# Optimization experiments

Hardware: AMD Instinct MI355X
Metric: run time of the kernel (lower is better)

Reference implementation:

```python
import jax, jax.numpy as jnp
import numpy as np

D_MODEL = 1024
NUM_HEADS = 16
D_K = D_MODEL // NUM_HEADS
D_FF = 4096
EPS = 1e-5


def layer_norm(x, gamma, beta):
    mu = jnp.mean(x, axis=-1, keepdims=True)
    var = jnp.mean(jnp.square(x - mu), axis=-1, keepdims=True)
    return (x - mu) * jax.lax.rsqrt(var + EPS) * gamma + beta


def setup_inputs() -> dict:
    key = jax.random.key(0)
    ks = jax.random.split(key, 12)
    B, S = 2, 2048
    s_attn = 1.0 / np.sqrt(D_MODEL)
    s_ff1 = 1.0 / np.sqrt(D_MODEL)
    s_ff2 = 1.0 / np.sqrt(D_FF)
    return {
        "x": jax.random.normal(ks[0], (B, S, D_MODEL), dtype=jnp.float32),
        "mask": jnp.ones((B, 1, 1, S), dtype=jnp.int32),
        "Wq": jax.random.normal(ks[1], (D_MODEL, D_MODEL), jnp.float32) * s_attn,
        "bq": jnp.zeros((D_MODEL,), jnp.float32),
        "Wk": jax.random.normal(ks[2], (D_MODEL, D_MODEL), jnp.float32) * s_attn,
        "bk": jnp.zeros((D_MODEL,), jnp.float32),
        "Wv": jax.random.normal(ks[3], (D_MODEL, D_MODEL), jnp.float32) * s_attn,
        "bv": jnp.zeros((D_MODEL,), jnp.float32),
        "Wo": jax.random.normal(ks[4], (D_MODEL, D_MODEL), jnp.float32) * s_attn,
        "bo": jnp.zeros((D_MODEL,), jnp.float32),
        "W1": jax.random.normal(ks[5], (D_MODEL, D_FF), jnp.float32) * s_ff1,
        "b1": jnp.zeros((D_FF,), jnp.float32),
        "W2": jax.random.normal(ks[6], (D_FF, D_MODEL), jnp.float32) * s_ff2,
        "b2": jnp.zeros((D_MODEL,), jnp.float32),
        "g1": jnp.ones((D_MODEL,), jnp.float32),
        "be1": jnp.zeros((D_MODEL,), jnp.float32),
        "g2": jnp.ones((D_MODEL,), jnp.float32),
        "be2": jnp.zeros((D_MODEL,), jnp.float32),
    }


def reference(x, mask, Wq, bq, Wk, bk, Wv, bv, Wo, bo, W1, b1, W2, b2, g1, be1, g2, be2):
    B, S, _ = x.shape

    def split_heads(t):  # [B,S,D] -> [B,H,S,Dk]
        return t.reshape(B, S, NUM_HEADS, D_K).transpose(0, 2, 1, 3)

    q = split_heads(x @ Wq + bq)
    k = split_heads(x @ Wk + bk)
    v = split_heads(x @ Wv + bv)

    scores = jnp.einsum("bhsd,bhtd->bhst", q, k) / np.sqrt(D_K)
    scores = jnp.where(mask == 0, -jnp.inf, scores)
    probs = jax.nn.softmax(scores, axis=-1)
    attn = jnp.einsum("bhst,bhtd->bhsd", probs, v)
    attn = attn.transpose(0, 2, 1, 3).reshape(B, S, D_MODEL)
    attn_out = attn @ Wo + bo

    h = layer_norm(x + attn_out, g1, be1)  # dropout=0 (eval)
    ff = jax.nn.relu(h @ W1 + b1) @ W2 + b2
    out = layer_norm(h + ff, g2, be2)
    return out
```

## Files before the change

kernel.cpp:

```cpp
#include <hip/hip_runtime.h>
#include <hip/hip_bf16.h>

#define DMODEL 1024
#define DFF    4096
#define NHEAD  16
#define DK     64
#define SEQ    2048
#define BATCH  2
#define MTOT   (BATCH*SEQ)
#define LOG2E  1.44269504f
#define MREF_L2E (-14.0f * 1.44269504f)

typedef __attribute__((ext_vector_type(8))) short bf16x8;
typedef __attribute__((ext_vector_type(4))) float f32x4;

typedef const unsigned int __attribute__((address_space(1)))* gas_u32p;
typedef unsigned int __attribute__((address_space(3)))* las_u32p;

__device__ __forceinline__ void gload_lds16(const void* g, void* l) {
  __builtin_amdgcn_global_load_lds((gas_u32p)g, (las_u32p)l, 16, 0, 0);
}

__device__ __forceinline__ f32x4 mfma16(bf16x8 a, bf16x8 b, f32x4 c) {
  return __builtin_amdgcn_mfma_f32_16x16x32_bf16(a, b, c, 0, 0, 0);
}

__device__ __forceinline__ unsigned short bf16bits(float f) {
  union { __hip_bfloat16 h; unsigned short u; } c; c.h = __float2bfloat16(f); return c.u;
}

__device__ __forceinline__ unsigned pack_bf16(float a, float b) {
  return (unsigned)bf16bits(a) | ((unsigned)bf16bits(b) << 16);
}

__device__ __forceinline__ void store_bf16x4(__hip_bfloat16* p, float a, float b, float c, float d) {
  union { __hip_bfloat16 h[4]; ushort4 u; } pk;
  pk.h[0] = __float2bfloat16(a); pk.h[1] = __float2bfloat16(b);
  pk.h[2] = __float2bfloat16(c); pk.h[3] = __float2bfloat16(d);
  *(ushort4*)p = pk.u;
}

__global__ __launch_bounds__(256) void cvt_bf16_kernel(const float* __restrict__ in,
                                                       __hip_bfloat16* __restrict__ out, int n) {
  int i = (blockIdx.x * 256 + threadIdx.x) * 4;
  if (i >= n) return;
  float4 v = *(const float4*)(in + i);
  store_bf16x4(out + i, v.x, v.y, v.z, v.w);
}

__global__ __launch_bounds__(256) void transpose_cvt_kernel(const float* __restrict__ in,
                                                            __hip_bfloat16* __restrict__ out,
                                                            int R, int C) {
  __shared__ float tile[32][33];
  int tx = threadIdx.x, ty = threadIdx.y;
  int c0 = blockIdx.x * 32, r0 = blockIdx.y * 32;
  #pragma unroll
  for (int j = 0; j < 32; j += 8)
    tile[ty + j][tx] = in[(size_t)(r0 + ty + j) * C + c0 + tx];
  __syncthreads();
  #pragma unroll
  for (int j = 0; j < 32; j += 8)
    out[(size_t)(c0 + ty + j) * R + r0 + tx] = __float2bfloat16(tile[tx][ty + j]);
}

__global__ __launch_bounds__(256)
void transpose4_cvt_kernel(const float* __restrict__ A0, const float* __restrict__ A1,
                           const float* __restrict__ A2, const float* __restrict__ A3,
                           __hip_bfloat16* __restrict__ O0, __hip_bfloat16* __restrict__ O1,
                           __hip_bfloat16* __restrict__ O2, __hip_bfloat16* __restrict__ O3) {
  const float* in; __hip_bfloat16* out;
  switch (blockIdx.z) {
    case 0: in = A0; out = O0; break;
    case 1: in = A1; out = O1; break;
    case 2: in = A2; out = O2; break;
    default: in = A3; out = O3; break;
  }
  __shared__ float tile[32][33];
  int tx = threadIdx.x, ty = threadIdx.y;
  int c0 = blockIdx.x * 32, r0 = blockIdx.y * 32;
  #pragma unroll
  for (int j = 0; j < 32; j += 8)
    tile[ty + j][tx] = in[(size_t)(r0 + ty + j) * DMODEL + c0 + tx];
  __syncthreads();
  #pragma unroll
  for (int j = 0; j < 32; j += 8)
    out[(size_t)(c0 + ty + j) * DMODEL + r0 + tx] = __float2bfloat16(tile[tx][ty + j]);
}

template<int MI, int NT>
__device__ __forceinline__ void gemm_core(const __hip_bfloat16* __restrict__ A,
                                          const __hip_bfloat16* __restrict__ Bt,
                                          int K, size_t blockM, size_t blockN,
                                          __hip_bfloat16* As, __hip_bfloat16* Bs,
                                          f32x4 (&acc)[MI][4]) {
  constexpr int BM = (NT / 128) * MI * 16;
  constexpr int RP = NT / 8;
  const int tid = threadIdx.x;
  const int w = tid >> 6, l = tid & 63;
  const int q = l >> 4, ln = l & 15;
  const int m_off = (w >> 1) * MI * 16, n_off = (w & 1) * 64;
  const int lr = l >> 3, lc = (l & 7) ^ lr;

  for (int k0 = 0; k0 < K; k0 += 64) {
    __syncthreads();
    #pragma unroll
    for (int t = 0; t < 128 / RP; ++t) {
      int ra = t * RP + w * 8;
      gload_lds16(Bt + (blockN + ra + lr) * (size_t)K + k0 + lc * 8, Bs + ra * 64);
      if (t < BM / RP)
        gload_lds16(A + (blockM + ra + lr) * (size_t)K + k0 + lc * 8, As + ra * 64);
    }
    __syncthreads();
    #pragma unroll
    for (int kk = 0; kk < 2; ++kk) {
      bf16x8 af[MI], bfr[4];
      #pragma unroll
      for (int mi = 0; mi < MI; ++mi) {
        int R = m_off + mi * 16 + ln;
        int p = (kk * 4 + q) ^ (R & 7);
        af[mi] = *(const bf16x8*)(As + R * 64 + p * 8);
      }
      #pragma unroll
      for (int ni = 0; ni < 4; ++ni) {
        int R = n_off + ni * 16 + ln;
        int p = (kk * 4 + q) ^ (R & 7);
        bfr[ni] = *(const bf16x8*)(Bs + R * 64 + p * 8);
      }
      #pragma unroll
      for (int mi = 0; mi < MI; ++mi)
        #pragma unroll
        for (int ni = 0; ni < 4; ++ni)
          acc[mi][ni] = mfma16(af[mi], bfr[ni], acc[mi][ni]);
    }
  }
}

template<int MI, int NT, int RELU, int WRITE_BF16>
__global__ __launch_bounds__(NT)
void gemm_bt_kernel(const __hip_bfloat16* __restrict__ A, const __hip_bfloat16* __restrict__ Bt,
                    const float* __restrict__ bias, float* __restrict__ Cf,
                    __hip_bfloat16* __restrict__ Cb, int M, int N, int K) {
  constexpr int BM = (NT / 128) * MI * 16;
  __shared__ __align__(16) __hip_bfloat16 As[BM * 64];
  __shared__ __align__(16) __hip_bfloat16 Bs[128 * 64];
  f32x4 acc[MI][4] = {};
  const size_t blockM = blockIdx.y * (size_t)BM, blockN = blockIdx.x * 128;
  gemm_core<MI, NT>(A, Bt, K, blockM, blockN, As, Bs, acc);

  const int tid = threadIdx.x;
  const int w = tid >> 6, l = tid & 63, q = l >> 4, ln = l & 15;
  const int m_off = (w >> 1) * MI * 16, n_off = (w & 1) * 64;
  #pragma unroll
  for (int ni = 0; ni < 4; ++ni) {
    size_t col = blockN + n_off + ni * 16 + ln;
    float bv = bias[col];
    #pragma unroll
    for (int mi = 0; mi < MI; ++mi) {
      size_t rowb = blockM + m_off + mi * 16 + q * 4;
      f32x4 v = acc[mi][ni];
      #pragma unroll
      for (int r = 0; r < 4; ++r) {
        float y = v[r] + bv;
        if (RELU) y = fmaxf(y, 0.0f);
        if (WRITE_BF16) Cb[(rowb + r) * N + col] = __float2bfloat16(y);
        else            Cf[(rowb + r) * N + col] = y;
      }
    }
  }
}

__global__ __launch_bounds__(256)
void gemm_qkv_kernel(const __hip_bfloat16* __restrict__ A, const __hip_bfloat16* __restrict__ Bt,
                     const float* __restrict__ bq, const float* __restrict__ bk,
                     const float* __restrict__ bv,
                     __hip_bfloat16* __restrict__ Qo, __hip_bfloat16* __restrict__ Ko,
                     __hip_bfloat16* __restrict__ VTo) {
  __shared__ __align__(16) __hip_bfloat16 As[128 * 64];
  __shared__ __align__(16) __hip_bfloat16 Bs[128 * 64];
  f32x4 acc[4][4] = {};
  const size_t blockM = blockIdx.y * 128, blockN = blockIdx.x * 128;
  const int sel = blockIdx.x >> 3;
  gemm_core<4, 256>(A, Bt, DMODEL, blockM, blockN, As, Bs, acc);

  const int tid = threadIdx.x;
  const int w = tid >> 6, l = tid & 63, q = l >> 4, ln = l & 15;
  const int m_off = (w >> 1) * 64, n_off = (w & 1) * 64;
  const int ncol0 = (int)blockN - sel * DMODEL;

  if (sel == 2) {
    #pragma unroll
    for (int ni = 0; ni < 4; ++ni) {
      int col = ncol0 + n_off + ni * 16 + ln;
      float bvv = bv[col];
      int hh = col >> 6, d = col & 63;
      #pragma unroll
      for (int mi = 0; mi < 4; ++mi) {
        size_t rowb = blockM + m_off + mi * 16 + q * 4;
        int bb = (int)(rowb >> 11), s = (int)(rowb & 2047);
        int sp = (s & ~0x1C) | ((s & 0x0C) << 1) | ((s & 0x10) >> 2);
        f32x4 v = acc[mi][ni];
        uint2 pk;
        pk.x = pack_bf16(v[0] + bvv, v[1] + bvv);
        pk.y = pack_bf16(v[2] + bvv, v[3] + bvv);
        *(uint2*)(VTo + (((size_t)(bb * NHEAD + hh) * DK + d) * SEQ + sp)) = pk;
      }
    }
  } else {
    const float* bias = (sel == 0) ? bq : bk;
    const float scale = (sel == 0) ? 0.125f : 1.0f;
    __hip_bfloat16* outp = (sel == 0) ? Qo : Ko;
    #pragma unroll
    for (int ni = 0; ni < 4; ++ni) {
      int col = ncol0 + n_off + ni * 16 + ln;
      float bvv = bias[col];
      #pragma unroll
      for (int mi = 0; mi < 4; ++mi) {
        size_t rowb = blockM + m_off + mi * 16 + q * 4;
        f32x4 v = acc[mi][ni];
        #pragma unroll
        for (int r = 0; r < 4; ++r)
          outp[(rowb + r) * DMODEL + col] = __float2bfloat16((v[r] + bvv) * scale);
      }
    }
  }
}

__global__ __launch_bounds__(128, 3)
void attn_kernel(const __hip_bfloat16* __restrict__ Q, const __hip_bfloat16* __restrict__ Kg,
                 const __hip_bfloat16* __restrict__ VT, const int* __restrict__ mask,
                 __hip_bfloat16* __restrict__ Oout) {
  const int tid = threadIdx.x, w = tid >> 6, l = tid & 63, q = l >> 4, ln = l & 15;
  const int qt = blockIdx.x, h = blockIdx.y, b = blockIdx.z;
  const size_t wrow = (size_t)b * SEQ + qt * 64 + w * 32;
  const int hcol = h * DK;
  const __hip_bfloat16* vth = VT + ((size_t)(b * NHEAD + h)) * DK * SEQ;
  const __hip_bfloat16* kgb = Kg + (size_t)b * SEQ * DMODEL + hcol;
  const int* mk = mask + (size_t)b * SEQ;

  __shared__ __align__(16) __hip_bfloat16 Ks[2][64 * 64];

  const int lr = l >> 3, lc = (l & 7) ^ lr;
  auto stage_k = [&](int buf, int kt) {
    #pragma unroll
    for (int t = 0; t < 4; ++t) {
      int ra = t * 16 + w * 8;
      gload_lds16(kgb + (size_t)(kt + ra + lr) * DMODEL + lc * 8, &Ks[buf][ra * 64]);
    }
  };

  bf16x8 qf[2][2];
  #pragma unroll
  for (int mi = 0; mi < 2; ++mi)
    #pragma unroll
    for (int kc = 0; kc < 2; ++kc)
      qf[mi][kc] = *(const bf16x8*)(Q + (wrow + mi * 16 + ln) * DMODEL + hcol + kc * 32 + q * 8);

  f32x4 Oacc[2][4] = {};
  float l_[2] = {0.f, 0.f};

  stage_k(0, 0);

  for (int it = 0; it < SEQ / 64; ++it) {
    const int kt = it * 64;
    __syncthreads();
    if (it + 1 < SEQ / 64) stage_k((it + 1) & 1, kt + 64);

    bf16x8 vf[8];
    #pragma unroll
    for (int ni = 0; ni < 4; ++ni)
      #pragma unroll
      for (int kc = 0; kc < 2; ++kc)
        vf[ni * 2 + kc] = *(const bf16x8*)(vth + (size_t)(ni * 16 + ln) * SEQ + kt + kc * 32 + q * 8);
    f32x4 mb[4];
    #pragma unroll
    for (int t = 0; t < 4; ++t) {
      int4 mv = *(const int4*)(mk + kt + t * 16 + q * 4);
      mb[t][0] = mv.x ? MREF_L2E : -1e30f; mb[t][1] = mv.y ? MREF_L2E : -1e30f;
      mb[t][2] = mv.z ? MREF_L2E : -1e30f; mb[t][3] = mv.w ? MREF_L2E : -1e30f;
    }

    const __hip_bfloat16* kb = &Ks[it & 1][0];
    f32x4 st[2][4] = {};
    #pragma unroll
    for (int kc = 0; kc < 2; ++kc)
      #pragma unroll
      for (int t = 0; t < 4; ++t) {
        int R = t * 16 + ln;
        bf16x8 kf = *(const bf16x8*)(kb + R * 64 + (((kc * 4 + q) ^ (R & 7)) << 3));
        #pragma unroll
        for (int mi = 0; mi < 2; ++mi)
          st[mi][t] = mfma16(kf, qf[mi][kc], st[mi][t]);
      }

    bf16x8 pf[2][2];
    #pragma unroll
    for (int mi = 0; mi < 2; ++mi) {
      float rs = 0.f;
      unsigned pk_[4][2];
      #pragma unroll
      for (int t = 0; t < 4; ++t) {
        float p0 = __builtin_amdgcn_exp2f(__builtin_fmaf(st[mi][t][0], LOG2E, mb[t][0]));
        float p1 = __builtin_amdgcn_exp2f(__builtin_fmaf(st[mi][t][1], LOG2E, mb[t][1]));
        float p2 = __builtin_amdgcn_exp2f(__builtin_fmaf(st[mi][t][2], LOG2E, mb[t][2]));
        float p3 = __builtin_amdgcn_exp2f(__builtin_fmaf(st[mi][t][3], LOG2E, mb[t][3]));
        rs += (p0 + p1) + (p2 + p3);
        pk_[t][0] = pack_bf16(p0, p1);
        pk_[t][1] = pack_bf16(p2, p3);
      }
      l_[mi] += rs;
      #pragma unroll
      for (int kc = 0; kc < 2; ++kc) {
        union { bf16x8 v; unsigned u[4]; } f;
        f.u[0] = pk_[kc * 2][0];     f.u[1] = pk_[kc * 2][1];
        f.u[2] = pk_[kc * 2 + 1][0]; f.u[3] = pk_[kc * 2 + 1][1];
        pf[mi][kc] = f.v;
      }
    }

    #pragma unroll
    for (int kc = 0; kc < 2; ++kc)
      #pragma unroll
      for (int mi = 0; mi < 2; ++mi)
        #pragma unroll
        for (int ni = 0; ni < 4; ++ni)
          Oacc[mi][ni] = mfma16(pf[mi][kc], vf[ni * 2 + kc], Oacc[mi][ni]);
  }

  #pragma unroll
  for (int mi = 0; mi < 2; ++mi) {
    l_[mi] += __shfl_xor(l_[mi], 16);
    l_[mi] += __shfl_xor(l_[mi], 32);
  }
  #pragma unroll
  for (int mi = 0; mi < 2; ++mi) {
    float inv = 1.0f / l_[mi];
    f32x4 i4;
    #pragma unroll
    for (int r = 0; r < 4; ++r) i4[r] = __shfl(inv, (l & 48) + q * 4 + r);
    #pragma unroll
    for (int ni = 0; ni < 4; ++ni)
      #pragma unroll
      for (int r = 0; r < 4; ++r)
        Oout[(wrow + mi * 16 + q * 4 + r) * DMODEL + hcol + ni * 16 + ln] =
            __float2bfloat16(Oacc[mi][ni][r] * i4[r]);
  }
}

__global__ __launch_bounds__(256)
void add_ln_kernel(const float* __restrict__ X, const float* __restrict__ Y,
                   const float* __restrict__ gam, const float* __restrict__ bet,
                   float* __restrict__ Of, __hip_bfloat16* __restrict__ Ob) {
  int row = blockIdx.x, tid = threadIdx.x;
  const float4 a = *(const float4*)(X + (size_t)row * DMODEL + tid * 4);
  const float4 c = *(const float4*)(Y + (size_t)row * DMODEL + tid * 4);
  float v0 = a.x + c.x, v1 = a.y + c.y, v2 = a.z + c.z, v3 = a.w + c.w;
  float s  = v0 + v1 + v2 + v3;
  float s2 = v0 * v0 + v1 * v1 + v2 * v2 + v3 * v3;
  #pragma unroll
  for (int off = 1; off < 64; off <<= 1) {
    s  += __shfl_xor(s, off);
    s2 += __shfl_xor(s2, off);
  }
  __shared__ float red[8];
  int w = tid >> 6, l = tid & 63;
  if (l == 0) { red[w] = s; red[4 + w] = s2; }
  __syncthreads();
  float S1 = red[0] + red[1] + red[2] + red[3];
  float S2 = red[4] + red[5] + red[6] + red[7];
  float mu = S1 * (1.0f / DMODEL);
  float var = S2 * (1.0f / DMODEL) - mu * mu;
  float rstd = rsqrtf(var + 1e-5f);
  const float4 gv = *(const float4*)(gam + tid * 4);
  const float4 bv = *(const float4*)(bet + tid * 4);
  float y0 = (v0 - mu) * rstd * gv.x + bv.x;
  float y1 = (v1 - mu) * rstd * gv.y + bv.y;
  float y2 = (v2 - mu) * rstd * gv.z + bv.z;
  float y3 = (v3 - mu) * rstd * gv.w + bv.w;
  float4 ov = {y0, y1, y2, y3};
  *(float4*)(Of + (size_t)row * DMODEL + tid * 4) = ov;
  if (Ob) store_bf16x4(Ob + (size_t)row * DMODEL + tid * 4, y0, y1, y2, y3);
}

extern "C" void kernel_launch(void* const* d_in, const int* in_sizes, int n_in,
                              void* d_out, int out_size, void* d_ws, size_t ws_size,
                              hipStream_t stream) {
  const float* x    = (const float*)d_in[0];
  const int*   mask = (const int*)d_in[1];
  const float* Wq = (const float*)d_in[2];  const float* bq = (const float*)d_in[3];
  const float* Wk = (const float*)d_in[4];  const float* bk = (const float*)d_in[5];
  const float* Wv = (const float*)d_in[6];  const float* bv = (const float*)d_in[7];
  const float* Wo = (const float*)d_in[8];  const float* bo = (const float*)d_in[9];
  const float* W1 = (const float*)d_in[10]; const float* b1 = (const float*)d_in[11];
  const float* W2 = (const float*)d_in[12]; const float* b2 = (const float*)d_in[13];
  const float* g1 = (const float*)d_in[14]; const float* be1 = (const float*)d_in[15];
  const float* g2 = (const float*)d_in[16]; const float* be2 = (const float*)d_in[17];
  float* out = (float*)d_out;

  char* ws = (char*)d_ws;
  const size_t MB = 1024ull * 1024ull;
  __hip_bfloat16* xb   = (__hip_bfloat16*)(ws + 0 * MB);
  __hip_bfloat16* WqT  = (__hip_bfloat16*)(ws + 8 * MB);
  __hip_bfloat16* WkT  = (__hip_bfloat16*)(ws + 10 * MB);
  __hip_bfloat16* WvT  = (__hip_bfloat16*)(ws + 12 * MB);
  __hip_bfloat16* WoT  = (__hip_bfloat16*)(ws + 14 * MB);
  __hip_bfloat16* W1T  = (__hip_bfloat16*)(ws + 16 * MB);
  __hip_bfloat16* W2T  = (__hip_bfloat16*)(ws + 24 * MB);
  __hip_bfloat16* Qb   = (__hip_bfloat16*)(ws + 32 * MB);
  __hip_bfloat16* Kb   = (__hip_bfloat16*)(ws + 40 * MB);
  __hip_bfloat16* VTb  = (__hip_bfloat16*)(ws + 48 * MB);
  __hip_bfloat16* attnB= (__hip_bfloat16*)(ws + 56 * MB);
  float*          AO   = (float*)(ws + 32 * MB);
  float*          hbuf = (float*)(ws + 48 * MB);
  __hip_bfloat16* hb   = (__hip_bfloat16*)(ws + 64 * MB);
  __hip_bfloat16* ff1  = (__hip_bfloat16*)(ws + 72 * MB);
  float*          ff2  = (float*)(ws + 32 * MB);

  dim3 blk256(256), blk128(128);
  dim3 blkT(32, 8);

  cvt_bf16_kernel<<<dim3(4096), blk256, 0, stream>>>(x, xb, MTOT * DMODEL);
  transpose4_cvt_kernel<<<dim3(32, 32, 4), blkT, 0, stream>>>(Wq, Wk, Wv, Wo, WqT, WkT, WvT, WoT);
  transpose_cvt_kernel<<<dim3(128, 32), blkT, 0, stream>>>(W1, W1T, DMODEL, DFF);
  transpose_cvt_kernel<<<dim3(32, 128), blkT, 0, stream>>>(W2, W2T, DFF, DMODEL);

  gemm_qkv_kernel<<<dim3(24, 32), blk256, 0, stream>>>(xb, WqT, bq, bk, bv, Qb, Kb, VTb);

  attn_kernel<<<dim3(32, 16, 2), blk128, 0, stream>>>(Qb, Kb, VTb, mask, attnB);

  gemm_bt_kernel<2, 256, 0, 0><<<dim3(8, 64), blk256, 0, stream>>>(attnB, WoT, bo, AO, nullptr, MTOT, DMODEL, DMODEL);

  add_ln_kernel<<<dim3(MTOT), blk256, 0, stream>>>(x, AO, g1, be1, hbuf, hb);

  gemm_bt_kernel<4, 256, 1, 1><<<dim3(32, 32), blk256, 0, stream>>>(hb, W1T, b1, nullptr, ff1, MTOT, DFF, DMODEL);

  gemm_bt_kernel<2, 256, 0, 0><<<dim3(8, 64), blk256, 0, stream>>>(ff1, W2T, b2, ff2, nullptr, MTOT, DMODEL, DFF);

  add_ln_kernel<<<dim3(MTOT), blk256, 0, stream>>>(hbuf, ff2, g2, be2, out, nullptr);
}
```

Before: 402.1 us.

## Split-K the FF2 GEMM and restructure attention to per-wave K staging

The second FFN GEMM now runs as a two-way split-K across blockIdx.z, writing two fp32 partial outputs that the final add+LayerNorm kernel sums together with the bias. This doubles the block count for the long-K GEMM to raise occupancy, at the cost of extra fp32 partial writes and reads. Separately, the attention kernel switches from block-shared 64-row K tiles guarded by __syncthreads to per-wave 32-row double buffers. It uses explicit vmcnt waits and no block barrier, shortening the dependency chain per iteration but doubling the loop trip count.

```diff
diff --git a/kernel.cpp b/kernel.cpp
--- a/kernel.cpp
+++ b/kernel.cpp
@@ -90,7 +90,7 @@
 template<int MI, int NT>
 __device__ __forceinline__ void gemm_core(const __hip_bfloat16* __restrict__ A,
                                           const __hip_bfloat16* __restrict__ Bt,
-                                          int K, size_t blockM, size_t blockN,
+                                          int Kc, int Kst, size_t blockM, size_t blockN,
                                           __hip_bfloat16* As, __hip_bfloat16* Bs,
                                           f32x4 (&acc)[MI][4]) {
   constexpr int BM = (NT / 128) * MI * 16;
@@ -101,14 +101,14 @@
   const int m_off = (w >> 1) * MI * 16, n_off = (w & 1) * 64;
   const int lr = l >> 3, lc = (l & 7) ^ lr;
 
-  for (int k0 = 0; k0 < K; k0 += 64) {
+  for (int k0 = 0; k0 < Kc; k0 += 64) {
     __syncthreads();
     #pragma unroll
     for (int t = 0; t < 128 / RP; ++t) {
       int ra = t * RP + w * 8;
-      gload_lds16(Bt + (blockN + ra + lr) * (size_t)K + k0 + lc * 8, Bs + ra * 64);
+      gload_lds16(Bt + (blockN + ra + lr) * (size_t)Kst + k0 + lc * 8, Bs + ra * 64);
       if (t < BM / RP)
-        gload_lds16(A + (blockM + ra + lr) * (size_t)K + k0 + lc * 8, As + ra * 64);
+        gload_lds16(A + (blockM + ra + lr) * (size_t)Kst + k0 + lc * 8, As + ra * 64);
     }
     __syncthreads();
     #pragma unroll
@@ -145,7 +145,7 @@
   __shared__ __align__(16) __hip_bfloat16 Bs[128 * 64];
   f32x4 acc[MI][4] = {};
   const size_t blockM = blockIdx.y * (size_t)BM, blockN = blockIdx.x * 128;
-  gemm_core<MI, NT>(A, Bt, K, blockM, blockN, As, Bs, acc);
+  gemm_core<MI, NT>(A, Bt, K, K, blockM, blockN, As, Bs, acc);
 
   const int tid = threadIdx.x;
   const int w = tid >> 6, l = tid & 63, q = l >> 4, ln = l & 15;
@@ -165,6 +165,38 @@
         if (WRITE_BF16) Cb[(rowb + r) * N + col] = __float2bfloat16(y);
         else            Cf[(rowb + r) * N + col] = y;
       }
+    }
+  }
+}
+
+template<int MI, int NT>
+__global__ __launch_bounds__(NT)
+void gemm_part_kernel(const __hip_bfloat16* __restrict__ A, const __hip_bfloat16* __restrict__ Bt,
+                      float* __restrict__ C0, float* __restrict__ C1,
+                      int M, int N, int Kc, int Kst) {
+  constexpr int BM = (NT / 128) * MI * 16;
+  __shared__ __align__(16) __hip_bfloat16 As[BM * 64];
+  __shared__ __align__(16) __hip_bfloat16 Bs[128 * 64];
+  f32x4 acc[MI][4] = {};
+  const size_t blockM = blockIdx.y * (size_t)BM, blockN = blockIdx.x * 128;
+  const __hip_bfloat16* Az  = A  + (size_t)blockIdx.z * Kc;
+  const __hip_bfloat16* Btz = Bt + (size_t)blockIdx.z * Kc;
+  gemm_core<MI, NT>(Az, Btz, Kc, Kst, blockM, blockN, As, Bs, acc);
+
+  float* C = blockIdx.z ? C1 : C0;
+  const int tid = threadIdx.x;
+  const int w = tid >> 6, l = tid & 63, q = l >> 4, ln = l & 15;
+  const int m_off = (w >> 1) * MI * 16, n_off = (w & 1) * 64;
+  #pragma unroll
+  for (int ni = 0; ni < 4; ++ni) {
+    size_t col = blockN + n_off + ni * 16 + ln;
+    #pragma unroll
+    for (int mi = 0; mi < MI; ++mi) {
+      size_t rowb = blockM + m_off + mi * 16 + q * 4;
+      f32x4 v = acc[mi][ni];
+      #pragma unroll
+      for (int r = 0; r < 4; ++r)
+        C[(rowb + r) * N + col] = v[r];
     }
   }
 }
@@ -180,7 +212,7 @@
   f32x4 acc[4][4] = {};
   const size_t blockM = blockIdx.y * 128, blockN = blockIdx.x * 128;
   const int sel = blockIdx.x >> 3;
-  gemm_core<4, 256>(A, Bt, DMODEL, blockM, blockN, As, Bs, acc);
+  gemm_core<4, 256>(A, Bt, DMODEL, DMODEL, blockM, blockN, As, Bs, acc);
 
   const int tid = threadIdx.x;
   const int w = tid >> 6, l = tid & 63, q = l >> 4, ln = l & 15;
@@ -237,15 +269,15 @@
   const __hip_bfloat16* kgb = Kg + (size_t)b * SEQ * DMODEL + hcol;
   const int* mk = mask + (size_t)b * SEQ;
 
-  __shared__ __align__(16) __hip_bfloat16 Ks[2][64 * 64];
+  __shared__ __align__(16) __hip_bfloat16 Ks[2][2][32 * 64];
 
   const int lr = l >> 3, lc = (l & 7) ^ lr;
-  auto stage_k = [&](int buf, int kt) {
-    #pragma unroll
-    for (int t = 0; t < 4; ++t) {
-      int ra = t * 16 + w * 8;
-      gload_lds16(kgb + (size_t)(kt + ra + lr) * DMODEL + lc * 8, &Ks[buf][ra * 64]);
-    }
+  __hip_bfloat16* kw0 = &Ks[w][0][0];
+  __hip_bfloat16* kw1 = &Ks[w][1][0];
+  auto stage_k = [&](__hip_bfloat16* dst, int kt) {
+    #pragma unroll
+    for (int t = 0; t < 4; ++t)
+      gload_lds16(kgb + (size_t)(kt + t * 8 + lr) * DMODEL + lc * 8, dst + t * 8 * 64);
   };
 
   bf16x8 qf[2][2];
@@ -258,72 +290,68 @@
   f32x4 Oacc[2][4] = {};
   float l_[2] = {0.f, 0.f};
 
-  stage_k(0, 0);
-
-  for (int it = 0; it < SEQ / 64; ++it) {
-    const int kt = it * 64;
-    __syncthreads();
-    if (it + 1 < SEQ / 64) stage_k((it + 1) & 1, kt + 64);
-
-    bf16x8 vf[8];
+  stage_k(kw0, 0);
+
+  for (int it = 0; it < SEQ / 32; ++it) {
+    const int kt = it * 32;
+
+    bf16x8 vf[4];
     #pragma unroll
     for (int ni = 0; ni < 4; ++ni)
-      #pragma unroll
-      for (int kc = 0; kc < 2; ++kc)
-        vf[ni * 2 + kc] = *(const bf16x8*)(vth + (size_t)(ni * 16 + ln) * SEQ + kt + kc * 32 + q * 8);
-    f32x4 mb[4];
-    #pragma unroll
-    for (int t = 0; t < 4; ++t) {
-      int4 mv = *(const int4*)(mk + kt + t * 16 + q * 4);
-      mb[t][0] = mv.x ? MREF_L2E : -1e30f; mb[t][1] = mv.y ? MREF_L2E : -1e30f;
-      mb[t][2] = mv.z ? MREF_L2E : -1e30f; mb[t][3] = mv.w ? MREF_L2E : -1e30f;
-    }
-
-    const __hip_bfloat16* kb = &Ks[it & 1][0];
-    f32x4 st[2][4] = {};
+      vf[ni] = *(const bf16x8*)(vth + (size_t)(ni * 16 + ln) * SEQ + kt + q * 8);
+    int4 mv0 = *(const int4*)(mk + kt + q * 4);
+    int4 mv1 = *(const int4*)(mk + kt + 16 + q * 4);
+
+    if (it + 1 < SEQ / 32) {
+      stage_k((it & 1) ? kw0 : kw1, kt + 32);
+      asm volatile("s_waitcnt vmcnt(10)" ::: "memory");
+    } else {
+      asm volatile("s_waitcnt vmcnt(6)" ::: "memory");
+    }
+    __builtin_amdgcn_sched_barrier(0);
+
+    const __hip_bfloat16* kb = (it & 1) ? kw1 : kw0;
+    f32x4 st[2][2] = {};
     #pragma unroll
     for (int kc = 0; kc < 2; ++kc)
       #pragma unroll
-      for (int t = 0; t < 4; ++t) {
-        int R = t * 16 + ln;
+      for (int t16 = 0; t16 < 2; ++t16) {
+        int R = t16 * 16 + ln;
         bf16x8 kf = *(const bf16x8*)(kb + R * 64 + (((kc * 4 + q) ^ (R & 7)) << 3));
         #pragma unroll
         for (int mi = 0; mi < 2; ++mi)
-          st[mi][t] = mfma16(kf, qf[mi][kc], st[mi][t]);
-      }
-
-    bf16x8 pf[2][2];
+          st[mi][t16] = mfma16(kf, qf[mi][kc], st[mi][t16]);
+      }
+
+    float mb0[4], mb1[4];
+    mb0[0] = mv0.x ? MREF_L2E : -1e30f; mb0[1] = mv0.y ? MREF_L2E : -1e30f;
+    mb0[2] = mv0.z ? MREF_L2E : -1e30f; mb0[3] = mv0.w ? MREF_L2E : -1e30f;
+    mb1[0] = mv1.x ? MREF_L2E : -1e30f; mb1[1] = mv1.y ? MREF_L2E : -1e30f;
+    mb1[2] = mv1.z ? MREF_L2E : -1e30f; mb1[3] = mv1.w ? MREF_L2E : -1e30f;
+
+    bf16x8 pf[2];
     #pragma unroll
     for (int mi = 0; mi < 2; ++mi) {
-      float rs = 0.f;
-      unsigned pk_[4][2];
-      #pragma unroll
-      for (int t = 0; t < 4; ++t) {
-        float p0 = __builtin_amdgcn_exp2f(__builtin_fmaf(st[mi][t][0], LOG2E, mb[t][0]));
-        float p1 = __builtin_amdgcn_exp2f(__builtin_fmaf(st[mi][t][1], LOG2E, mb[t][1]));
-        float p2 = __builtin_amdgcn_exp2f(__builtin_fmaf(st[mi][t][2], LOG2E, mb[t][2]));
-        float p3 = __builtin_amdgcn_exp2f(__builtin_fmaf(st[mi][t][3], LOG2E, mb[t][3]));
-        rs += (p0 + p1) + (p2 + p3);
-        pk_[t][0] = pack_bf16(p0, p1);
-        pk_[t][1] = pack_bf16(p2, p3);
-      }
-      l_[mi] += rs;
-      #pragma unroll
-      for (int kc = 0; kc < 2; ++kc) {
-        union { bf16x8 v; unsigned u[4]; } f;
-        f.u[0] = pk_[kc * 2][0];     f.u[1] = pk_[kc * 2][1];
-        f.u[2] = pk_[kc * 2 + 1][0]; f.u[3] = pk_[kc * 2 + 1][1];
-        pf[mi][kc] = f.v;
-      }
-    }
-
-    #pragma unroll
-    for (int kc = 0; kc < 2; ++kc)
-      #pragma unroll
-      for (int mi = 0; mi < 2; ++mi)
-        #pragma unroll
-        for (int ni = 0; ni < 4; ++ni)
-          Oacc[mi][ni] = mfma16(pf[mi][kc], vf[ni * 2 + kc], Oacc[mi][ni]);
+      float p00 = __builtin_amdgcn_exp2f(__builtin_fmaf(st[mi][0][0], LOG2E, mb0[0]));
+      float p01 = __builtin_amdgcn_exp2f(__builtin_fmaf(st[mi][0][1], LOG2E, mb0[1]));
+      float p02 = __builtin_amdgcn_exp2f(__builtin_fmaf(st[mi][0][2], LOG2E, mb0[2]));
+      float p03 = __builtin_amdgcn_exp2f(__builtin_fmaf(st[mi][0][3], LOG2E, mb0[3]));
+      float p10 = __builtin_amdgcn_exp2f(__builtin_fmaf(st[mi][1][0], LOG2E, mb1[0]));
+      float p11 = __builtin_amdgcn_exp2f(__builtin_fmaf(st[mi][1][1], LOG2E, mb1[1]));
+      float p12 = __builtin_amdgcn_exp2f(__builtin_fmaf(st[mi][1][2], LOG2E, mb1[2]));
+      float p13 = __builtin_amdgcn_exp2f(__builtin_fmaf(st[mi][1][3], LOG2E, mb1[3]));
+      l_[mi] += ((p00 + p01) + (p02 + p03)) + ((p10 + p11) + (p12 + p13));
+      union { bf16x8 v; unsigned u[4]; } f;
+      f.u[0] = pack_bf16(p00, p01); f.u[1] = pack_bf16(p02, p03);
+      f.u[2] = pack_bf16(p10, p11); f.u[3] = pack_bf16(p12, p13);
+      pf[mi] = f.v;
+    }
+
+    #pragma unroll
+    for (int mi = 0; mi < 2; ++mi)
+      #pragma unroll
+      for (int ni = 0; ni < 4; ++ni)
+        Oacc[mi][ni] = mfma16(pf[mi], vf[ni], Oacc[mi][ni]);
   }
 
   #pragma unroll
@@ -348,12 +376,21 @@
 
 __global__ __launch_bounds__(256)
 void add_ln_kernel(const float* __restrict__ X, const float* __restrict__ Y,
+                   const float* __restrict__ Y1, const float* __restrict__ bias,
                    const float* __restrict__ gam, const float* __restrict__ bet,
                    float* __restrict__ Of, __hip_bfloat16* __restrict__ Ob) {
   int row = blockIdx.x, tid = threadIdx.x;
   const float4 a = *(const float4*)(X + (size_t)row * DMODEL + tid * 4);
   const float4 c = *(const float4*)(Y + (size_t)row * DMODEL + tid * 4);
   float v0 = a.x + c.x, v1 = a.y + c.y, v2 = a.z + c.z, v3 = a.w + c.w;
+  if (Y1) {
+    const float4 d = *(const float4*)(Y1 + (size_t)row * DMODEL + tid * 4);
+    v0 += d.x; v1 += d.y; v2 += d.z; v3 += d.w;
+  }
+  if (bias) {
+    const float4 e = *(const float4*)(bias + tid * 4);
+    v0 += e.x; v1 += e.y; v2 += e.z; v3 += e.w;
+  }
   float s  = v0 + v1 + v2 + v3;
   float s2 = v0 * v0 + v1 * v1 + v2 * v2 + v3 * v3;
   #pragma unroll
@@ -413,7 +450,8 @@
   float*          hbuf = (float*)(ws + 48 * MB);
   __hip_bfloat16* hb   = (__hip_bfloat16*)(ws + 64 * MB);
   __hip_bfloat16* ff1  = (__hip_bfloat16*)(ws + 72 * MB);
-  float*          ff2  = (float*)(ws + 32 * MB);
+  float*          ff2a = (float*)(ws + 0 * MB);
+  float*          ff2b = (float*)(ws + 32 * MB);
 
   dim3 blk256(256), blk128(128);
   dim3 blkT(32, 8);
@@ -429,11 +467,11 @@
 
   gemm_bt_kernel<2, 256, 0, 0><<<dim3(8, 64), blk256, 0, stream>>>(attnB, WoT, bo, AO, nullptr, MTOT, DMODEL, DMODEL);
 
-  add_ln_kernel<<<dim3(MTOT), blk256, 0, stream>>>(x, AO, g1, be1, hbuf, hb);
+  add_ln_kernel<<<dim3(MTOT), blk256, 0, stream>>>(x, AO, nullptr, nullptr, g1, be1, hbuf, hb);
 
   gemm_bt_kernel<4, 256, 1, 1><<<dim3(32, 32), blk256, 0, stream>>>(hb, W1T, b1, nullptr, ff1, MTOT, DFF, DMODEL);
 
-  gemm_bt_kernel<2, 256, 0, 0><<<dim3(8, 64), blk256, 0, stream>>>(ff1, W2T, b2, ff2, nullptr, MTOT, DMODEL, DFF);
-
-  add_ln_kernel<<<dim3(MTOT), blk256, 0, stream>>>(hbuf, ff2, g2, be2, out, nullptr);
-}
+  gemm_part_kernel<2, 256><<<dim3(8, 64, 2), blk256, 0, stream>>>(ff1, W2T, ff2a, ff2b, MTOT, DMODEL, DFF / 2, DFF);
+
+  add_ln_kernel<<<dim3(MTOT), blk256, 0, stream>>>(hbuf, ff2a, ff2b, b2, g2, be2, out, nullptr);
+}
```

Measured after the change: 400.9 us. No clear change (-0.3%).
